# Kernel tuning notes

Measured on AMD Instinct MI355X. Metric: run time of the kernel, lower is better.

## Reference

```python
import jax, jax.numpy as jnp
import numpy as np

D = 512       # d_model
M = 64        # working memory_dim
SE = 32       # episodic slots
SS = 64       # semantic slots
H = 4         # episodic heads
B, L = 2, 1024
BOT = max(D // 4, 32)  # controller bottleneck = 128


def _layernorm(x, g, b, eps=1e-5):
    mu = jnp.mean(x, axis=-1, keepdims=True)
    var = jnp.var(x, axis=-1, keepdims=True)
    return (x - mu) * jax.lax.rsqrt(var + eps) * g + b


def setup_inputs() -> dict:
    key = jax.random.key(0)
    ks = jax.random.split(key, 24)
    r = lambda i, shape, s=0.02: jax.random.normal(ks[i], shape, dtype=jnp.float32) * s
    return {
        "x": jax.random.normal(ks[0], (B, L, D), dtype=jnp.float32),
        # WorkingMemory (weights stored as (in, out))
        "Wq": r(1, (D, M)), "Wk": r(2, (D, M)), "Wv": r(3, (D, D)),
        "Wf": r(4, (D, M)), "bf": jnp.zeros((M,), jnp.float32),
        "Wo": r(5, (D, D)),
        "ln_g": jnp.ones((D,), jnp.float32), "ln_b": jnp.zeros((D,), jnp.float32),
        # EpisodicMemory
        "eslots": r(6, (1, SE, D)),
        "Eq": r(7, (D, D)), "Ek": r(8, (D, D)), "Ev": r(9, (D, D)), "Eo": r(10, (D, D)),
        # SemanticMemory
        "know": r(11, (1, SS, D)),
        "Sin": r(12, (D, D)),
        "Sg_w": r(13, (D, D)), "Sg_b": jnp.zeros((D,), jnp.float32),
        "So": r(14, (D, D)),
        # MemoryController
        "C1w": r(15, (D, BOT)), "C1b": jnp.zeros((BOT,), jnp.float32),
        "C2w": r(16, (BOT, 3)), "C2b": jnp.zeros((3,), jnp.float32),
    }


def _forward(x, Wq, Wk, Wv, Wf, bf, Wo, ln_g, ln_b,
             eslots, Eq, Ek, Ev, Eo,
             know, Sin, Sg_w, Sg_b, So,
             C1w, C1b, C2w, C2b):
    b, l, d = x.shape
    # ---- WorkingMemory (parallel gated linear attention) ----
    scale = M ** -0.5
    q = (jax.nn.elu(x @ Wq) + 1.0) * scale          # (B,L,M)
    k = jax.nn.elu(x @ Wk) + 1.0                    # (B,L,M)
    v = x @ Wv                                      # (B,L,D)
    forget = jax.nn.sigmoid(x @ Wf + bf)            # (B,L,M)
    log_f_cum = jnp.clip(jnp.cumsum(jnp.log(jnp.clip(forget, 1e-6, None)), axis=1), -20.0, 20.0)
    exp_neg = jnp.exp(-log_f_cum)
    exp_pos = jnp.exp(log_f_cum)
    kv = k[..., :, None] * v[..., None, :]          # (B,L,M,D) outer product
    cum_kv = jnp.cumsum(exp_neg[..., None] * kv, axis=1)
    Mstate = exp_pos[..., None] * cum_kv            # (B,L,M,D)
    z = exp_pos * jnp.cumsum(exp_neg * k, axis=1)   # (B,L,M)
    num = jnp.einsum('blm,blmd->bld', q, Mstate)
    den = jnp.einsum('blm,blm->bl', q, z)[..., None] + 1e-6
    w_out = _layernorm(num / den, ln_g, ln_b) @ Wo  # (B,L,D)

    # ---- EpisodicMemory (cross-attn to learned slots) ----
    hd = D // H
    mem = jnp.broadcast_to(eslots, (b, SE, D))
    qh = (x @ Eq).reshape(b, l, H, hd)
    kh = (mem @ Ek).reshape(b, SE, H, hd)
    vh = (mem @ Ev).reshape(b, SE, H, hd)
    scores = jnp.einsum('blhe,bshe->bhls', qh, kh) / jnp.sqrt(jnp.float32(hd))
    attn = jax.nn.softmax(scores, axis=-1)
    e_out = jnp.einsum('bhls,bshe->blhe', attn, vh).reshape(b, l, D) @ Eo

    # ---- SemanticMemory (single-head attn to knowledge, gated residual) ----
    kb = jnp.broadcast_to(know, (b, SS, D))
    qs = x @ Sin                                    # (B,L,D)
    s_scores = jnp.einsum('bld,bsd->bls', qs, kb) / jnp.sqrt(jnp.float32(D))
    s_attn = jax.nn.softmax(s_scores, axis=-1)
    retrieved = jnp.einsum('bls,bsd->bld', s_attn, kb)
    gate = jax.nn.sigmoid(x @ Sg_w + Sg_b)
    s_out = (gate * retrieved + (1.0 - gate) * x) @ So

    # ---- Controller fusion ----
    wts = jax.nn.softmax(jax.nn.silu(x @ C1w + C1b) @ C2w + C2b, axis=-1)  # (B,L,3)
    fused = (wts[..., 0:1] * w_out + wts[..., 1:2] * e_out + wts[..., 2:3] * s_out)
    return fused


def reference(x, Wq, Wk, Wv, Wf, bf, Wo, ln_g, ln_b,
              eslots, Eq, Ek, Ev, Eo,
              know, Sin, Sg_w, Sg_b, So,
              C1w, C1b, C2w, C2b):
    return _forward(x, Wq, Wk, Wv, Wf, bf, Wo, ln_g, ln_b,
                    eslots, Eq, Ek, Ev, Eo,
                    know, Sin, Sg_w, Sg_b, So,
                    C1w, C1b, C2w, C2b)
```

## Files before the change

kernel.cpp:

```cpp
#include <hip/hip_runtime.h>
#include <cstdint>

typedef unsigned int uint;
typedef unsigned short ushort;
typedef __attribute__((ext_vector_type(8))) short bf16x8;
typedef __attribute__((ext_vector_type(4))) float f32x4;

__device__ __forceinline__ ushort f2b(float f) {
  union { float f; uint u; } v; v.f = f;
  uint u = v.u;
  uint r = (u + 0x7FFFu + ((u >> 16) & 1u)) >> 16;
  return (ushort)r;
}
__device__ __forceinline__ float b2f(ushort h) {
  union { uint u; float f; } v; v.u = ((uint)h) << 16; return v.f;
}

__global__ __launch_bounds__(256) void k_prep(
    const float* __restrict__ x, const float* __restrict__ Wv, const float* __restrict__ Sg,
    const float* __restrict__ C1w, const float* __restrict__ Wq, const float* __restrict__ Wk,
    const float* __restrict__ Wo, const float* __restrict__ So, const float* __restrict__ know,
    const float* __restrict__ eslots, const float* __restrict__ Ek, const float* __restrict__ Ev,
    const float* __restrict__ Sin, const float* __restrict__ Wf, const float* __restrict__ bfb,
    ushort* __restrict__ X16, ushort* __restrict__ Wcat, ushort* __restrict__ Wfin,
    ushort* __restrict__ know16, float* __restrict__ kh, float* __restrict__ vh,
    float* __restrict__ logfb)
{
  __shared__ __align__(16) float Af[16 * 32];
  __shared__ __align__(16) float Bf[32 * 64];
  int bid = blockIdx.x;
  int tid = threadIdx.x;

  if (bid < 1024) {
    int t = bid * 256 + tid;
    float4 xv = *(const float4*)&x[(size_t)t * 4];
    uint p01 = (uint)f2b(xv.x) | ((uint)f2b(xv.y) << 16);
    uint p23 = (uint)f2b(xv.z) | ((uint)f2b(xv.w) << 16);
    uint2 o; o.x = p01; o.y = p23;
    *(uint2*)&X16[(size_t)t * 4] = o;
    return;
  }
  if (bid < 5760) {
    int i = (bid - 1024) * 256 + tid;
    if (i < 262144) { int n = i >> 9, k = i & 511; Wcat[n * 512 + k] = f2b(Wv[k * 512 + n]); return; }
    i -= 262144;
    if (i < 262144) { int n = i >> 9, k = i & 511; Wcat[(704 + n) * 512 + k] = f2b(Sg[k * 512 + n]); return; }
    i -= 262144;
    if (i < 65536) { int n = i >> 9, k = i & 511; Wcat[(1216 + n) * 512 + k] = f2b(C1w[k * 128 + n]); return; }
    i -= 65536;
    if (i < 32768) { int n = i >> 9, k = i & 511; Wcat[(1344 + n) * 512 + k] = f2b(Wq[k * 64 + n]); return; }
    i -= 32768;
    if (i < 32768) { int n = i >> 9, k = i & 511; Wcat[(1408 + n) * 512 + k] = f2b(Wk[k * 64 + n]); return; }
    i -= 32768;
    if (i < 262144) { int n = i >> 9, k = i & 511; Wfin[n * 1152 + k] = f2b(Wo[k * 512 + n]); return; }
    i -= 262144;
    if (i < 262144) { int n = i >> 9, k = i & 511; Wfin[n * 1152 + 512 + k] = f2b(So[k * 512 + n]); return; }
    i -= 262144;
    know16[i] = f2b(know[i]);
    return;
  }
  if (bid < 6016) {
    int t = (bid - 5760) * 256 + tid;
    if (t < 16384) {
      int s = t >> 9, j = t & 511;
      float acc = 0.f;
      #pragma unroll 8
      for (int d = 0; d < 512; ++d) acc += eslots[s * 512 + d] * Ek[d * 512 + j];
      kh[s * 512 + j] = acc;
    } else if (t < 32768) {
      int o = t - 16384; int s = o >> 9, j = o & 511;
      float acc = 0.f;
      #pragma unroll 8
      for (int d = 0; d < 512; ++d) acc += eslots[s * 512 + d] * Ev[d * 512 + j];
      vh[s * 512 + j] = acc;
    } else {
      int o = t - 32768; int k = o >> 6, s = o & 63;
      float acc = 0.f;
      #pragma unroll 8
      for (int d = 0; d < 512; ++d) acc += Sin[k * 512 + d] * know[s * 512 + d];
      Wcat[(640 + s) * 512 + k] = f2b(acc * 0.04419417382415922f);
    }
    return;
  }
  {
    int r0 = (bid - 6016) * 16;
    int row = tid >> 4, col4 = (tid & 15) * 4;
    float a0 = 0.f, a1 = 0.f, a2 = 0.f, a3 = 0.f;
    for (int kt = 0; kt < 16; ++kt) {
      if (tid < 128) {
        int p = tid; int rr = p >> 3, c4 = (p & 7) * 4;
        *(float4*)&Af[rr * 32 + c4] = *(const float4*)&x[(size_t)(r0 + rr) * 512 + kt * 32 + c4];
      }
      #pragma unroll
      for (int i = 0; i < 2; ++i) {
        int p = i * 256 + tid; int rr = p >> 4, c4 = (p & 15) * 4;
        *(float4*)&Bf[rr * 64 + c4] = *(const float4*)&Wf[(size_t)(kt * 32 + rr) * 64 + c4];
      }
      __syncthreads();
      #pragma unroll 8
      for (int ks = 0; ks < 32; ++ks) {
        float a = Af[row * 32 + ks];
        float4 b = *(float4*)&Bf[ks * 64 + col4];
        a0 += a * b.x; a1 += a * b.y; a2 += a * b.z; a3 += a * b.w;
      }
      __syncthreads();
    }
    float accs[4] = {a0, a1, a2, a3};
    #pragma unroll
    for (int j = 0; j < 4; ++j) {
      float logit = accs[j] + bfb[col4 + j];
      float s = 1.f / (1.f + expf(-logit));
      logfb[(size_t)(r0 + row) * 64 + col4 + j] = logf(fmaxf(s, 1e-6f));
    }
  }
}

__global__ __launch_bounds__(256) void k_pre2(
    const float* __restrict__ Eq, const float* __restrict__ kh, const float* __restrict__ vh,
    const float* __restrict__ Eo, ushort* __restrict__ Wcat, ushort* __restrict__ Wfin)
{
  int t = blockIdx.x * 256 + threadIdx.x;
  if (t < 65536) {
    int k = t >> 7, hs = t & 127; int h = hs >> 5, s = hs & 31;
    const float* eqp = Eq + k * 512 + h * 128;
    const float* khp = kh + s * 512 + h * 128;
    float acc = 0.f;
    #pragma unroll 8
    for (int e = 0; e < 128; ++e) acc += eqp[e] * khp[e];
    Wcat[(512 + hs) * 512 + k] = f2b(acc * 0.08838834764831845f);
  } else {
    int o = t - 65536; int hs = o >> 9, j = o & 511; int h = hs >> 5, s = hs & 31;
    const float* vhp = vh + s * 512 + h * 128;
    float acc = 0.f;
    #pragma unroll 8
    for (int e = 0; e < 128; ++e) acc += vhp[e] * Eo[(h * 128 + e) * 512 + j];
    Wfin[j * 1152 + 1024 + hs] = f2b(acc);
  }
}

__global__ __launch_bounds__(256) void k_gemm1(
    const ushort* __restrict__ A, const ushort* __restrict__ Bw, float* __restrict__ C,
    const float* __restrict__ sgb, const float* __restrict__ c1b)
{
  __shared__ __align__(16) ushort As[64 * 32];
  __shared__ __align__(16) ushort Bs[128 * 32];
  int tid = threadIdx.x;
  int lane = tid & 63, wv = tid >> 6;
  int wm = (wv & 1) * 32, wn = (wv >> 1) * 64;
  int lr = lane & 15, lk = lane >> 4;
  int m0 = blockIdx.y * 64, n0 = blockIdx.x * 128;
  f32x4 zero4 = {0.f, 0.f, 0.f, 0.f};
  f32x4 acc[2][4];
  #pragma unroll
  for (int a = 0; a < 2; ++a)
    #pragma unroll
    for (int b = 0; b < 4; ++b) acc[a][b] = zero4;
  for (int kt = 0; kt < 16; ++kt) {
    int k0 = kt * 32;
    {
      int p = tid, row = p >> 2, cc = p & 3;
      int cs = cc ^ ((row >> 1) & 3);
      *(uint4*)&As[p * 8] = *(const uint4*)&A[(size_t)(m0 + row) * 512 + k0 + cs * 8];
    }
    #pragma unroll
    for (int i = 0; i < 2; ++i) {
      int p = i * 256 + tid, row = p >> 2, cc = p & 3;
      int cs = cc ^ ((row >> 1) & 3);
      *(uint4*)&Bs[p * 8] = *(const uint4*)&Bw[(size_t)(n0 + row) * 512 + k0 + cs * 8];
    }
    __syncthreads();
    bf16x8 af[2], bfv[4];
    #pragma unroll
    for (int mi = 0; mi < 2; ++mi) {
      int row = wm + mi * 16 + lr;
      int cc = lk ^ ((row >> 1) & 3);
      af[mi] = *(bf16x8*)&As[row * 32 + cc * 8];
    }
    #pragma unroll
    for (int ni = 0; ni < 4; ++ni) {
      int row = wn + ni * 16 + lr;
      int cc = lk ^ ((row >> 1) & 3);
      bfv[ni] = *(bf16x8*)&Bs[row * 32 + cc * 8];
    }
    #pragma unroll
    for (int mi = 0; mi < 2; ++mi)
      #pragma unroll
      for (int ni = 0; ni < 4; ++ni)
        acc[mi][ni] = __builtin_amdgcn_mfma_f32_16x16x32_bf16(af[mi], bfv[ni], acc[mi][ni], 0, 0, 0);
    __syncthreads();
  }
  #pragma unroll
  for (int mi = 0; mi < 2; ++mi) {
    #pragma unroll
    for (int ni = 0; ni < 4; ++ni) {
      int col = n0 + wn + ni * 16 + lr;
      #pragma unroll
      for (int r = 0; r < 4; ++r) {
        int rowb = m0 + wm + mi * 16 + lk * 4 + r;
        float v = acc[mi][ni][r];
        if (col >= 704) {
          if (col < 1216) { v = 1.f / (1.f + __expf(-(v + sgb[col - 704]))); }
          else if (col < 1344) { float tt = v + c1b[col - 1216]; v = tt / (1.f + __expf(-tt)); }
          else if (col < 1408) { float e = (v > 0.f) ? v : (__expf(v) - 1.f); v = (e + 1.f) * 0.125f; }
          else if (col < 1472) { float e = (v > 0.f) ? v : (__expf(v) - 1.f); v = e + 1.f; }
        }
        C[(size_t)rowb * 1536 + col] = v;
      }
    }
  }
}

__global__ __launch_bounds__(256) void k_gemm2(
    const ushort* __restrict__ A, const ushort* __restrict__ Bw, float* __restrict__ C)
{
  __shared__ __align__(16) ushort As[64 * 32];
  __shared__ __align__(16) ushort Bs[64 * 32];
  int tid = threadIdx.x;
  int lane = tid & 63, wv = tid >> 6;
  int wm = (wv & 1) * 32, wn = (wv >> 1) * 32;
  int lr = lane & 15, lk = lane >> 4;
  int m0 = blockIdx.y * 64, n0 = blockIdx.x * 64;
  f32x4 zero4 = {0.f, 0.f, 0.f, 0.f};
  f32x4 acc[2][2];
  #pragma unroll
  for (int a = 0; a < 2; ++a)
    #pragma unroll
    for (int b = 0; b < 2; ++b) acc[a][b] = zero4;
  for (int kt = 0; kt < 36; ++kt) {
    int k0 = kt * 32;
    {
      int p = tid, row = p >> 2, cc = p & 3;
      int cs = cc ^ ((row >> 1) & 3);
      *(uint4*)&As[p * 8] = *(const uint4*)&A[(size_t)(m0 + row) * 1152 + k0 + cs * 8];
      *(uint4*)&Bs[p * 8] = *(const uint4*)&Bw[(size_t)(n0 + row) * 1152 + k0 + cs * 8];
    }
    __syncthreads();
    bf16x8 af[2], bfv[2];
    #pragma unroll
    for (int mi = 0; mi < 2; ++mi) {
      int row = wm + mi * 16 + lr;
      int cc = lk ^ ((row >> 1) & 3);
      af[mi] = *(bf16x8*)&As[row * 32 + cc * 8];
    }
    #pragma unroll
    for (int ni = 0; ni < 2; ++ni) {
      int row = wn + ni * 16 + lr;
      int cc = lk ^ ((row >> 1) & 3);
      bfv[ni] = *(bf16x8*)&Bs[row * 32 + cc * 8];
    }
    #pragma unroll
    for (int mi = 0; mi < 2; ++mi)
      #pragma unroll
      for (int ni = 0; ni < 2; ++ni)
        acc[mi][ni] = __builtin_amdgcn_mfma_f32_16x16x32_bf16(af[mi], bfv[ni], acc[mi][ni], 0, 0, 0);
    __syncthreads();
  }
  #pragma unroll
  for (int mi = 0; mi < 2; ++mi) {
    #pragma unroll
    for (int ni = 0; ni < 2; ++ni) {
      int col = n0 + wn + ni * 16 + lr;
      #pragma unroll
      for (int r = 0; r < 4; ++r) {
        int rowb = m0 + wm + mi * 16 + lk * 4 + r;
        C[(size_t)rowb * 512 + col] = acc[mi][ni][r];
      }
    }
  }
}

__global__ __launch_bounds__(256) void k_gatescan(
    const float* __restrict__ logfb, const float* __restrict__ P,
    float* __restrict__ cn, float* __restrict__ qe, float* __restrict__ qz)
{
  __shared__ float wsumA[4];
  __shared__ float wsumB[4];
  int bidx = blockIdx.x;
  int b = bidx >> 6, m = bidx & 63;
  int tid = threadIdx.x;
  int lane = tid & 63, wv = tid >> 6;
  size_t rbase = (size_t)b * 1024 + tid * 4;

  float v0 = logfb[(rbase + 0) * 64 + m];
  float v1 = logfb[(rbase + 1) * 64 + m];
  float v2 = logfb[(rbase + 2) * 64 + m];
  float v3 = logfb[(rbase + 3) * 64 + m];
  v1 += v0; v2 += v1; v3 += v2;
  float tsum = v3;
  float sc = tsum;
  #pragma unroll
  for (int o = 1; o < 64; o <<= 1) {
    float t = __shfl_up(sc, o, 64);
    if (lane >= o) sc += t;
  }
  if (lane == 63) wsumA[wv] = sc;
  __syncthreads();
  float excl = sc - tsum;
  #pragma unroll
  for (int w2 = 0; w2 < 3; ++w2) if (w2 < wv) excl += wsumA[w2];

  float vv[4] = {v0, v1, v2, v3};
  float cv[4], qv[4];
  #pragma unroll
  for (int i = 0; i < 4; ++i) {
    size_t r = rbase + i;
    float lf = fminf(fmaxf(excl + vv[i], -20.f), 20.f);
    float en = expf(-lf), ep = expf(lf);
    float kk = P[r * 1536 + 1408 + m];
    float qq = P[r * 1536 + 1344 + m];
    cv[i] = en * kk;
    qv[i] = qq * ep;
    cn[r * 64 + m] = cv[i];
    qe[r * 64 + m] = qv[i];
  }

  float c1 = cv[0], c2 = c1 + cv[1], c3 = c2 + cv[2], c4 = c3 + cv[3];
  float t2 = c4;
  float sc2 = t2;
  #pragma unroll
  for (int o = 1; o < 64; o <<= 1) {
    float t = __shfl_up(sc2, o, 64);
    if (lane >= o) sc2 += t;
  }
  if (lane == 63) wsumB[wv] = sc2;
  __syncthreads();
  float excl2 = sc2 - t2;
  #pragma unroll
  for (int w2 = 0; w2 < 3; ++w2) if (w2 < wv) excl2 += wsumB[w2];

  float pr[4] = {c1, c2, c3, c4};
  #pragma unroll
  for (int i = 0; i < 4; ++i) {
    size_t r = rbase + i;
    qz[r * 64 + m] = qv[i] * (excl2 + pr[i]);
  }
}

__global__ __launch_bounds__(256) void k_scanA(
    const float* __restrict__ cn, const float* __restrict__ P, float* __restrict__ Send)
{
  __shared__ __align__(16) float cnS[16 * 64];
  __shared__ __align__(16) float vS[16 * 64];
  int tid = threadIdx.x;
  int bid = blockIdx.x;
  int dt = bid & 7, c = (bid >> 3) & 15, b = bid >> 7;
  int rb0 = b * 1024 + c * 64;
  int mg = tid >> 4, dl = tid & 15;
  float4 acc[4];
  #pragma unroll
  for (int i = 0; i < 4; ++i) acc[i] = make_float4(0.f, 0.f, 0.f, 0.f);
  for (int ig = 0; ig < 4; ++ig) {
    int rb = rb0 + ig * 16;
    int row = tid >> 4, c4f = (tid & 15) * 4;
    *(float4*)&cnS[row * 64 + c4f] = *(const float4*)&cn[(size_t)(rb + row) * 64 + c4f];
    *(float4*)&vS[row * 64 + c4f] = *(const float4*)&P[(size_t)(rb + row) * 1536 + dt * 64 + c4f];
    __syncthreads();
    #pragma unroll 4
    for (int i = 0; i < 16; ++i) {
      float4 vv = *(float4*)&vS[i * 64 + dl * 4];
      float4 cm = *(float4*)&cnS[i * 64 + mg * 4];
      acc[0].x += cm.x * vv.x; acc[0].y += cm.x * vv.y; acc[0].z += cm.x * vv.z; acc[0].w += cm.x * vv.w;
      acc[1].x += cm.y * vv.x; acc[1].y += cm.y * vv.y; acc[1].z += cm.y * vv.z; acc[1].w += cm.y * vv.w;
      acc[2].x += cm.z * vv.x; acc[2].y += cm.z * vv.y; acc[2].z += cm.z * vv.z; acc[2].w += cm.z * vv.w;
      acc[3].x += cm.w * vv.x; acc[3].y += cm.w * vv.y; acc[3].z += cm.w * vv.z; acc[3].w += cm.w * vv.w;
    }
    __syncthreads();
  }
  #pragma unroll
  for (int mi = 0; mi < 4; ++mi) {
    int m = mg * 4 + mi;
    *(float4*)&Send[(size_t)((b * 16 + c) * 64 + m) * 512 + dt * 64 + dl * 4] = acc[mi];
  }
}

__global__ __launch_bounds__(256) void k_scanB(const float* __restrict__ Send, float* __restrict__ carry)
{
  int t = blockIdx.x * 256 + threadIdx.x;
  int d = t & 511, m = (t >> 9) & 63, b = t >> 15;
  float run = 0.f;
  for (int c = 0; c < 16; ++c) {
    size_t idx = (size_t)((b * 16 + c) * 64 + m) * 512 + d;
    carry[idx] = run;
    run += Send[idx];
  }
}

__global__ __launch_bounds__(256) void k_scanC(
    const float* __restrict__ cn, const float* __restrict__ qe, const float* __restrict__ P,
    const float* __restrict__ carry, float* __restrict__ num)
{
  __shared__ __align__(16) float cnS[16 * 64];
  __shared__ __align__(16) float qeS[16 * 64];
  __shared__ __align__(16) float vS[16 * 64];
  int tid = threadIdx.x;
  int bid = blockIdx.x;
  int dt = bid & 7, c = (bid >> 3) & 15, b = bid >> 7;
  int rb0 = b * 1024 + c * 64;
  int mg = tid & 3, dl = tid >> 2;
  int d = dt * 64 + dl;
  float S[16];
  #pragma unroll
  for (int mi = 0; mi < 16; ++mi)
    S[mi] = carry[(size_t)((b * 16 + c) * 64 + mg * 16 + mi) * 512 + d];
  for (int ig = 0; ig < 4; ++ig) {
    int rb = rb0 + ig * 16;
    int row = tid >> 4, c4f = (tid & 15) * 4;
    *(float4*)&cnS[row * 64 + c4f] = *(const float4*)&cn[(size_t)(rb + row) * 64 + c4f];
    *(float4*)&qeS[row * 64 + c4f] = *(const float4*)&qe[(size_t)(rb + row) * 64 + c4f];
    *(float4*)&vS[row * 64 + c4f] = *(const float4*)&P[(size_t)(rb + row) * 1536 + dt * 64 + c4f];
    __syncthreads();
    for (int i = 0; i < 16; ++i) {
      float vv = vS[i * 64 + dl];
      float p = 0.f;
      #pragma unroll
      for (int j = 0; j < 4; ++j) {
        float4 c4 = *(float4*)&cnS[i * 64 + mg * 16 + j * 4];
        float4 q4 = *(float4*)&qeS[i * 64 + mg * 16 + j * 4];
        S[j * 4 + 0] += c4.x * vv; p += q4.x * S[j * 4 + 0];
        S[j * 4 + 1] += c4.y * vv; p += q4.y * S[j * 4 + 1];
        S[j * 4 + 2] += c4.z * vv; p += q4.z * S[j * 4 + 2];
        S[j * 4 + 3] += c4.w * vv; p += q4.w * S[j * 4 + 3];
      }
      p += __shfl_xor(p, 1);
      p += __shfl_xor(p, 2);
      if (mg == 0) num[(size_t)(rb + i) * 512 + d] = p;
    }
    __syncthreads();
  }
}

__global__ __launch_bounds__(256) void k_post(
    const float* __restrict__ P, const float* __restrict__ x,
    const float* __restrict__ num, const float* __restrict__ qz,
    const ushort* __restrict__ know16, const float* __restrict__ lng,
    const float* __restrict__ lnb, const float* __restrict__ C2w,
    const float* __restrict__ C2b, ushort* __restrict__ Afin)
{
  __shared__ __align__(16) ushort kbuf[32 * 512];
  __shared__ float attnL[4][64];
  __shared__ float w2L[4];
  int tid = threadIdx.x;
  int w = tid >> 6, lane = tid & 63;
  int r0 = blockIdx.x * 4;
  int r = r0 + w;
  size_t pr = (size_t)r * 1536;

  float h0 = P[pr + 1216 + lane], h1 = P[pr + 1280 + lane];
  float a0 = h0 * C2w[lane * 3 + 0] + h1 * C2w[(64 + lane) * 3 + 0];
  float a1 = h0 * C2w[lane * 3 + 1] + h1 * C2w[(64 + lane) * 3 + 1];
  float a2 = h0 * C2w[lane * 3 + 2] + h1 * C2w[(64 + lane) * 3 + 2];
  #pragma unroll
  for (int o = 32; o; o >>= 1) {
    a0 += __shfl_xor(a0, o); a1 += __shfl_xor(a1, o); a2 += __shfl_xor(a2, o);
  }
  a0 += C2b[0]; a1 += C2b[1]; a2 += C2b[2];
  float mxc = fmaxf(a0, fmaxf(a1, a2));
  float e0 = expf(a0 - mxc), e1 = expf(a1 - mxc), e2c = expf(a2 - mxc);
  float inv = 1.f / (e0 + e1 + e2c);
  float w0 = e0 * inv, w1 = e1 * inv, w2 = e2c * inv;
  if (lane == 0) w2L[w] = w2;

  {
    float den = qz[(size_t)r * 64 + lane];
    #pragma unroll
    for (int o = 32; o; o >>= 1) den += __shfl_xor(den, o);
    den += 1e-6f;
    float y[8];
    float4 n0 = *(const float4*)&num[(size_t)r * 512 + lane * 8];
    float4 n1 = *(const float4*)&num[(size_t)r * 512 + lane * 8 + 4];
    y[0] = n0.x / den; y[1] = n0.y / den; y[2] = n0.z / den; y[3] = n0.w / den;
    y[4] = n1.x / den; y[5] = n1.y / den; y[6] = n1.z / den; y[7] = n1.w / den;
    float s1 = 0.f, s2 = 0.f;
    #pragma unroll
    for (int i = 0; i < 8; ++i) { s1 += y[i]; s2 += y[i] * y[i]; }
    #pragma unroll
    for (int o = 32; o; o >>= 1) { s1 += __shfl_xor(s1, o); s2 += __shfl_xor(s2, o); }
    float mu = s1 * (1.f / 512.f);
    float var = s2 * (1.f / 512.f) - mu * mu;
    float rs = rsqrtf(var + 1e-5f);
    uint4 outv;
    uint pk[4];
    #pragma unroll
    for (int p2 = 0; p2 < 4; ++p2) {
      float o0 = (y[2 * p2] - mu) * rs * lng[lane * 8 + 2 * p2] + lnb[lane * 8 + 2 * p2];
      float o1 = (y[2 * p2 + 1] - mu) * rs * lng[lane * 8 + 2 * p2 + 1] + lnb[lane * 8 + 2 * p2 + 1];
      pk[p2] = (uint)f2b(o0 * w0) | ((uint)f2b(o1 * w0) << 16);
    }
    outv.x = pk[0]; outv.y = pk[1]; outv.z = pk[2]; outv.w = pk[3];
    *(uint4*)&Afin[(size_t)r * 1152 + lane * 8] = outv;
  }

  {
    int h = lane >> 4, ei = (lane & 15) * 2;
    float v0 = P[pr + 512 + h * 32 + ei], v1 = P[pr + 512 + h * 32 + ei + 1];
    float mxe = fmaxf(v0, v1);
    #pragma unroll
    for (int o = 1; o < 16; o <<= 1) mxe = fmaxf(mxe, __shfl_xor(mxe, o));
    float ee0 = __expf(v0 - mxe), ee1 = __expf(v1 - mxe);
    float ss = ee0 + ee1;
    #pragma unroll
    for (int o = 1; o < 16; o <<= 1) ss += __shfl_xor(ss, o);
    float sc1 = w1 / ss;
    uint pkv = (uint)f2b(ee0 * sc1) | ((uint)f2b(ee1 * sc1) << 16);
    *(uint*)&Afin[(size_t)r * 1152 + 1024 + h * 32 + ei] = pkv;
  }

  {
    float lv = P[pr + 640 + lane];
    float mx = lv;
    #pragma unroll
    for (int o = 32; o; o >>= 1) mx = fmaxf(mx, __shfl_xor(mx, o));
    float e = __expf(lv - mx);
    float sum = e;
    #pragma unroll
    for (int o = 32; o; o >>= 1) sum += __shfl_xor(sum, o);
    attnL[w][lane] = e / sum;
  }

  int dd = tid * 2;
  float acc[4][2];
  #pragma unroll
  for (int i = 0; i < 4; ++i) { acc[i][0] = 0.f; acc[i][1] = 0.f; }
  for (int hs = 0; hs < 2; ++hs) {
    #pragma unroll
    for (int i = 0; i < 8; ++i) {
      int idx = i * 256 + tid;
      *(uint4*)&kbuf[idx * 8] = *(const uint4*)&know16[(size_t)hs * 16384 + idx * 8];
    }
    __syncthreads();
    for (int s = 0; s < 32; ++s) {
      uint uu = *(uint*)&kbuf[s * 512 + dd];
      float k0 = b2f((ushort)(uu & 0xffff));
      float k1 = b2f((ushort)(uu >> 16));
      #pragma unroll
      for (int row = 0; row < 4; ++row) {
        float a = attnL[row][hs * 32 + s];
        acc[row][0] += a * k0;
        acc[row][1] += a * k1;
      }
    }
    __syncthreads();
  }
  #pragma unroll
  for (int row = 0; row < 4; ++row) {
    int rr = r0 + row;
    float g0 = P[(size_t)rr * 1536 + 704 + dd];
    float g1 = P[(size_t)rr * 1536 + 704 + dd + 1];
    float x0 = x[(size_t)rr * 512 + dd], x1 = x[(size_t)rr * 512 + dd + 1];
    float w2v = w2L[row];
    float m0 = g0 * acc[row][0] + (1.f - g0) * x0;
    float m1 = g1 * acc[row][1] + (1.f - g1) * x1;
    uint pkv = (uint)f2b(w2v * m0) | ((uint)f2b(w2v * m1) << 16);
    *(uint*)&Afin[(size_t)rr * 1152 + 512 + dd] = pkv;
  }
}

extern "C" void kernel_launch(void* const* d_in, const int* in_sizes, int n_in,
                              void* d_out, int out_size, void* d_ws, size_t ws_size,
                              hipStream_t stream)
{
  const float* x     = (const float*)d_in[0];
  const float* Wq    = (const float*)d_in[1];
  const float* Wk    = (const float*)d_in[2];
  const float* Wv    = (const float*)d_in[3];
  const float* Wf    = (const float*)d_in[4];
  const float* bfb   = (const float*)d_in[5];
  const float* Wo    = (const float*)d_in[6];
  const float* ln_g  = (const float*)d_in[7];
  const float* ln_b  = (const float*)d_in[8];
  const float* eslots= (const float*)d_in[9];
  const float* Eq    = (const float*)d_in[10];
  const float* Ek    = (const float*)d_in[11];
  const float* Ev    = (const float*)d_in[12];
  const float* Eo    = (const float*)d_in[13];
  const float* know  = (const float*)d_in[14];
  const float* Sin   = (const float*)d_in[15];
  const float* Sg_w  = (const float*)d_in[16];
  const float* Sg_b  = (const float*)d_in[17];
  const float* So    = (const float*)d_in[18];
  const float* C1w   = (const float*)d_in[19];
  const float* C1b   = (const float*)d_in[20];
  const float* C2w   = (const float*)d_in[21];
  const float* C2b   = (const float*)d_in[22];

  char* ws = (char*)d_ws;
  ushort* X16    = (ushort*)(ws + 0);
  ushort* Wcat   = (ushort*)(ws + 2097152);
  ushort* Wfin   = (ushort*)(ws + 3670016);
  ushort* know16 = (ushort*)(ws + 4849664);
  float*  kh     = (float*)(ws + 4915200);
  float*  vh     = (float*)(ws + 4980736);
  float*  P      = (float*)(ws + 5046272);
  float*  logfb  = (float*)(ws + 17629184);
  float*  cn     = (float*)(ws + 18153472);
  float*  qe     = (float*)(ws + 18677760);
  float*  qz     = (float*)(ws + 19202048);
  float*  Send   = (float*)(ws + 19726336);
  float*  carry  = (float*)(ws + 23920640);
  float*  num    = (float*)(ws + 28114944);
  ushort* Afin   = (ushort*)(ws + 32342016);

  k_prep<<<dim3(6144), dim3(256), 0, stream>>>(x, Wv, Sg_w, C1w, Wq, Wk, Wo, So, know,
                                               eslots, Ek, Ev, Sin, Wf, bfb,
                                               X16, Wcat, Wfin, know16, kh, vh, logfb);
  k_pre2<<<dim3(512), dim3(256), 0, stream>>>(Eq, kh, vh, Eo, Wcat, Wfin);
  k_gemm1<<<dim3(12, 32), dim3(256), 0, stream>>>(X16, Wcat, P, Sg_b, C1b);
  k_gatescan<<<dim3(128), dim3(256), 0, stream>>>(logfb, P, cn, qe, qz);
  k_scanA<<<dim3(256), dim3(256), 0, stream>>>(cn, P, Send);
  k_scanB<<<dim3(256), dim3(256), 0, stream>>>(Send, carry);
  k_scanC<<<dim3(256), dim3(256), 0, stream>>>(cn, qe, P, carry, num);
  k_post<<<dim3(512), dim3(256), 0, stream>>>(P, x, num, qz, know16, ln_g, ln_b, C2w, C2b, Afin);
  k_gemm2<<<dim3(8, 32), dim3(256), 0, stream>>>(Afin, Wfin, (float*)d_out);
}
```

Baseline: 150.8 us.

## Coalesce weight transposes via shared-memory tiles and warp-reduce small dot products

The prep kernel replaces its element-wise strided weight transposes with 64x64 shared-memory tiled transposes that write packed bf16 in 16-byte stores. The Sin·know and Eq·kh products move from one thread per output with strided serial loops to one wavefront per row, using coalesced loads and shuffle reductions. The x and know bf16 conversions are grid-strided over fewer blocks, and the grid shrinks from 6144 to 816 blocks, with the long-running forget-gate GEMM blocks scheduled first. The aim is to remove uncoalesced global accesses and launch overhead in the preprocessing stage.

```diff
diff --git a/kernel.cpp b/kernel.cpp
--- a/kernel.cpp
+++ b/kernel.cpp
@@ -28,89 +28,134 @@
 {
   __shared__ __align__(16) float Af[16 * 32];
   __shared__ __align__(16) float Bf[32 * 64];
+  __shared__ __align__(16) float T[64][65];
   int bid = blockIdx.x;
   int tid = threadIdx.x;
-
-  if (bid < 1024) {
-    int t = bid * 256 + tid;
-    float4 xv = *(const float4*)&x[(size_t)t * 4];
-    uint p01 = (uint)f2b(xv.x) | ((uint)f2b(xv.y) << 16);
-    uint p23 = (uint)f2b(xv.z) | ((uint)f2b(xv.w) << 16);
-    uint2 o; o.x = p01; o.y = p23;
-    *(uint2*)&X16[(size_t)t * 4] = o;
+  int lane = tid & 63, wv = tid >> 6;
+
+  if (bid < 128) {
+    int r0 = bid * 16;
+    int row = tid >> 4, col4 = (tid & 15) * 4;
+    float a0 = 0.f, a1 = 0.f, a2 = 0.f, a3 = 0.f;
+    for (int kt = 0; kt < 16; ++kt) {
+      if (tid < 128) {
+        int p = tid; int rr = p >> 3, c4 = (p & 7) * 4;
+        *(float4*)&Af[rr * 32 + c4] = *(const float4*)&x[(size_t)(r0 + rr) * 512 + kt * 32 + c4];
+      }
+      #pragma unroll
+      for (int i = 0; i < 2; ++i) {
+        int p = i * 256 + tid; int rr = p >> 4, c4 = (p & 15) * 4;
+        *(float4*)&Bf[rr * 64 + c4] = *(const float4*)&Wf[(size_t)(kt * 32 + rr) * 64 + c4];
+      }
+      __syncthreads();
+      #pragma unroll 8
+      for (int ks = 0; ks < 32; ++ks) {
+        float a = Af[row * 32 + ks];
+        float4 b = *(float4*)&Bf[ks * 64 + col4];
+        a0 += a * b.x; a1 += a * b.y; a2 += a * b.z; a3 += a * b.w;
+      }
+      __syncthreads();
+    }
+    float accs[4] = {a0, a1, a2, a3};
+    #pragma unroll
+    for (int j = 0; j < 4; ++j) {
+      float logit = accs[j] + bfb[col4 + j];
+      float s = 1.f / (1.f + expf(-logit));
+      logfb[(size_t)(r0 + row) * 64 + col4 + j] = logf(fmaxf(s, 1e-6f));
+    }
     return;
   }
-  if (bid < 5760) {
-    int i = (bid - 1024) * 256 + tid;
-    if (i < 262144) { int n = i >> 9, k = i & 511; Wcat[n * 512 + k] = f2b(Wv[k * 512 + n]); return; }
-    i -= 262144;
-    if (i < 262144) { int n = i >> 9, k = i & 511; Wcat[(704 + n) * 512 + k] = f2b(Sg[k * 512 + n]); return; }
-    i -= 262144;
-    if (i < 65536) { int n = i >> 9, k = i & 511; Wcat[(1216 + n) * 512 + k] = f2b(C1w[k * 128 + n]); return; }
-    i -= 65536;
-    if (i < 32768) { int n = i >> 9, k = i & 511; Wcat[(1344 + n) * 512 + k] = f2b(Wq[k * 64 + n]); return; }
-    i -= 32768;
-    if (i < 32768) { int n = i >> 9, k = i & 511; Wcat[(1408 + n) * 512 + k] = f2b(Wk[k * 64 + n]); return; }
-    i -= 32768;
-    if (i < 262144) { int n = i >> 9, k = i & 511; Wfin[n * 1152 + k] = f2b(Wo[k * 512 + n]); return; }
-    i -= 262144;
-    if (i < 262144) { int n = i >> 9, k = i & 511; Wfin[n * 1152 + 512 + k] = f2b(So[k * 512 + n]); return; }
-    i -= 262144;
-    know16[i] = f2b(know[i]);
-    return;
-  }
-  if (bid < 6016) {
-    int t = (bid - 5760) * 256 + tid;
+  if (bid < 256) {
+    int t = (bid - 128) * 256 + tid;
     if (t < 16384) {
       int s = t >> 9, j = t & 511;
       float acc = 0.f;
       #pragma unroll 8
       for (int d = 0; d < 512; ++d) acc += eslots[s * 512 + d] * Ek[d * 512 + j];
       kh[s * 512 + j] = acc;
-    } else if (t < 32768) {
+    } else {
       int o = t - 16384; int s = o >> 9, j = o & 511;
       float acc = 0.f;
       #pragma unroll 8
       for (int d = 0; d < 512; ++d) acc += eslots[s * 512 + d] * Ev[d * 512 + j];
       vh[s * 512 + j] = acc;
-    } else {
-      int o = t - 32768; int k = o >> 6, s = o & 63;
-      float acc = 0.f;
-      #pragma unroll 8
-      for (int d = 0; d < 512; ++d) acc += Sin[k * 512 + d] * know[s * 512 + d];
-      Wcat[(640 + s) * 512 + k] = f2b(acc * 0.04419417382415922f);
     }
     return;
   }
+  if (bid < 384) {
+    int k = (bid - 256) * 4 + wv;
+    const float* sp = Sin + (size_t)k * 512 + lane * 8;
+    float4 s1 = *(const float4*)&sp[0];
+    float4 s2 = *(const float4*)&sp[4];
+    for (int s = 0; s < 64; ++s) {
+      const float* kp = know + (size_t)s * 512 + lane * 8;
+      float4 k1 = *(const float4*)&kp[0];
+      float4 k2 = *(const float4*)&kp[4];
+      float part = s1.x * k1.x + s1.y * k1.y + s1.z * k1.z + s1.w * k1.w
+                 + s2.x * k2.x + s2.y * k2.y + s2.z * k2.z + s2.w * k2.w;
+      #pragma unroll
+      for (int o = 32; o; o >>= 1) part += __shfl_xor(part, o);
+      if (lane == 0) Wcat[(640 + s) * 512 + k] = f2b(part * 0.04419417382415922f);
+    }
+    return;
+  }
+  if (bid < 672) {
+    int tt = bid - 384;
+    const float* src; ushort* dst; int sld, dld, Nt, drow, dcol;
+    if (tt < 64)       {           src = Wv;  dst = Wcat; sld = 512; dld = 512;  Nt = 8; drow = 0;    dcol = 0;   }
+    else if (tt < 128) { tt -= 64; src = Sg;  dst = Wcat; sld = 512; dld = 512;  Nt = 8; drow = 704;  dcol = 0;   }
+    else if (tt < 144) { tt -= 128; src = C1w; dst = Wcat; sld = 128; dld = 512; Nt = 2; drow = 1216; dcol = 0;   }
+    else if (tt < 152) { tt -= 144; src = Wq;  dst = Wcat; sld = 64;  dld = 512; Nt = 1; drow = 1344; dcol = 0;   }
+    else if (tt < 160) { tt -= 152; src = Wk;  dst = Wcat; sld = 64;  dld = 512; Nt = 1; drow = 1408; dcol = 0;   }
+    else if (tt < 224) { tt -= 160; src = Wo;  dst = Wfin; sld = 512; dld = 1152; Nt = 8; drow = 0;   dcol = 0;   }
+    else               { tt -= 224; src = So;  dst = Wfin; sld = 512; dld = 1152; Nt = 8; drow = 0;   dcol = 512; }
+    int tk = tt / Nt, tn = tt % Nt;
+    int k0 = tk * 64, n0 = tn * 64;
+    int r = tid >> 4, c = (tid & 15) * 4;
+    #pragma unroll
+    for (int p = 0; p < 4; ++p) {
+      int kk = p * 16 + r;
+      float4 v = *(const float4*)&src[(size_t)(k0 + kk) * sld + n0 + c];
+      T[c + 0][kk] = v.x; T[c + 1][kk] = v.y; T[c + 2][kk] = v.z; T[c + 3][kk] = v.w;
+    }
+    __syncthreads();
+    int n = tid >> 2, kc = (tid & 3) * 16;
+    uint u[8];
+    #pragma unroll
+    for (int j = 0; j < 8; ++j) {
+      ushort lo = f2b(T[n][kc + 2 * j]);
+      ushort hi = f2b(T[n][kc + 2 * j + 1]);
+      u[j] = (uint)lo | ((uint)hi << 16);
+    }
+    size_t off = (size_t)(drow + n0 + n) * dld + dcol + k0 + kc;
+    uint4 o1; o1.x = u[0]; o1.y = u[1]; o1.z = u[2]; o1.w = u[3];
+    uint4 o2; o2.x = u[4]; o2.y = u[5]; o2.z = u[6]; o2.w = u[7];
+    *(uint4*)&dst[off] = o1;
+    *(uint4*)&dst[off + 8] = o2;
+    return;
+  }
+  if (bid < 800) {
+    int base = (bid - 672) * 256 + tid;
+    #pragma unroll
+    for (int it = 0; it < 8; ++it) {
+      int t = base + it * 32768;
+      float4 xv = *(const float4*)&x[(size_t)t * 4];
+      uint2 o;
+      o.x = (uint)f2b(xv.x) | ((uint)f2b(xv.y) << 16);
+      o.y = (uint)f2b(xv.z) | ((uint)f2b(xv.w) << 16);
+      *(uint2*)&X16[(size_t)t * 4] = o;
+    }
+    return;
+  }
   {
-    int r0 = (bid - 6016) * 16;
-    int row = tid >> 4, col4 = (tid & 15) * 4;
-    float a0 = 0.f, a1 = 0.f, a2 = 0.f, a3 = 0.f;
-    for (int kt = 0; kt < 16; ++kt) {
-      if (tid < 128) {
-        int p = tid; int rr = p >> 3, c4 = (p & 7) * 4;
-        *(float4*)&Af[rr * 32 + c4] = *(const float4*)&x[(size_t)(r0 + rr) * 512 + kt * 32 + c4];
-      }
-      #pragma unroll
-      for (int i = 0; i < 2; ++i) {
-        int p = i * 256 + tid; int rr = p >> 4, c4 = (p & 15) * 4;
-        *(float4*)&Bf[rr * 64 + c4] = *(const float4*)&Wf[(size_t)(kt * 32 + rr) * 64 + c4];
-      }
-      __syncthreads();
-      #pragma unroll 8
-      for (int ks = 0; ks < 32; ++ks) {
-        float a = Af[row * 32 + ks];
-        float4 b = *(float4*)&Bf[ks * 64 + col4];
-        a0 += a * b.x; a1 += a * b.y; a2 += a * b.z; a3 += a * b.w;
-      }
-      __syncthreads();
-    }
-    float accs[4] = {a0, a1, a2, a3};
-    #pragma unroll
-    for (int j = 0; j < 4; ++j) {
-      float logit = accs[j] + bfb[col4 + j];
-      float s = 1.f / (1.f + expf(-logit));
-      logfb[(size_t)(r0 + row) * 64 + col4 + j] = logf(fmaxf(s, 1e-6f));
+    int t = (bid - 800) * 256 + tid;
+    #pragma unroll
+    for (int j = 0; j < 2; ++j) {
+      float4 v = *(const float4*)&know[(size_t)t * 8 + j * 4];
+      uint2 o;
+      o.x = (uint)f2b(v.x) | ((uint)f2b(v.y) << 16);
+      o.y = (uint)f2b(v.z) | ((uint)f2b(v.w) << 16);
+      *(uint2*)&know16[(size_t)t * 8 + j * 4] = o;
     }
   }
 }
@@ -119,22 +164,34 @@
     const float* __restrict__ Eq, const float* __restrict__ kh, const float* __restrict__ vh,
     const float* __restrict__ Eo, ushort* __restrict__ Wcat, ushort* __restrict__ Wfin)
 {
-  int t = blockIdx.x * 256 + threadIdx.x;
-  if (t < 65536) {
-    int k = t >> 7, hs = t & 127; int h = hs >> 5, s = hs & 31;
-    const float* eqp = Eq + k * 512 + h * 128;
-    const float* khp = kh + s * 512 + h * 128;
+  int bid = blockIdx.x;
+  int tid = threadIdx.x;
+  int lane = tid & 63, wv = tid >> 6;
+  if (bid < 256) {
+    int gw = bid * 4 + wv;
+    #pragma unroll
+    for (int pp = 0; pp < 2; ++pp) {
+      int pair = gw * 2 + pp;
+      int k = pair >> 2, h = pair & 3;
+      const float* ep = Eq + (size_t)k * 512 + h * 128 + lane * 2;
+      float e0 = ep[0], e1 = ep[1];
+      for (int s = 0; s < 32; ++s) {
+        const float* kp = kh + (size_t)s * 512 + h * 128 + lane * 2;
+        float part = e0 * kp[0] + e1 * kp[1];
+        #pragma unroll
+        for (int o = 32; o; o >>= 1) part += __shfl_xor(part, o);
+        if (lane == 0) Wcat[(512 + h * 32 + s) * 512 + k] = f2b(part * 0.08838834764831845f);
+      }
+    }
+  } else {
+    int o = (bid - 256) * 256 + tid;
+    int hs = o >> 9, j = o & 511;
+    int h = hs >> 5, s = hs & 31;
+    const float* vhp = vh + (size_t)s * 512 + h * 128;
     float acc = 0.f;
     #pragma unroll 8
-    for (int e = 0; e < 128; ++e) acc += eqp[e] * khp[e];
-    Wcat[(512 + hs) * 512 + k] = f2b(acc * 0.08838834764831845f);
-  } else {
-    int o = t - 65536; int hs = o >> 9, j = o & 511; int h = hs >> 5, s = hs & 31;
-    const float* vhp = vh + s * 512 + h * 128;
-    float acc = 0.f;
-    #pragma unroll 8
-    for (int e = 0; e < 128; ++e) acc += vhp[e] * Eo[(h * 128 + e) * 512 + j];
-    Wfin[j * 1152 + 1024 + hs] = f2b(acc);
+    for (int e = 0; e < 128; ++e) acc += vhp[e] * Eo[(size_t)(h * 128 + e) * 512 + j];
+    Wfin[(size_t)j * 1152 + 1024 + hs] = f2b(acc);
   }
 }
 
@@ -600,9 +657,9 @@
   float*  num    = (float*)(ws + 28114944);
   ushort* Afin   = (ushort*)(ws + 32342016);
 
-  k_prep<<<dim3(6144), dim3(256), 0, stream>>>(x, Wv, Sg_w, C1w, Wq, Wk, Wo, So, know,
-                                               eslots, Ek, Ev, Sin, Wf, bfb,
-                                               X16, Wcat, Wfin, know16, kh, vh, logfb);
+  k_prep<<<dim3(816), dim3(256), 0, stream>>>(x, Wv, Sg_w, C1w, Wq, Wk, Wo, So, know,
+                                              eslots, Ek, Ev, Sin, Wf, bfb,
+                                              X16, Wcat, Wfin, know16, kh, vh, logfb);
   k_pre2<<<dim3(512), dim3(256), 0, stream>>>(Eq, kh, vh, Eo, Wcat, Wfin);
   k_gemm1<<<dim3(12, 32), dim3(256), 0, stream>>>(X16, Wcat, P, Sg_b, C1b);
   k_gatescan<<<dim3(128), dim3(256), 0, stream>>>(logfb, P, cn, qe, qz);
```

After: 145.3 us. -3.6%, faster.
